# Kernel optimization log

Measured on AMD Instinct MI355X. Metric: run time of the kernel, lower is better.

The kernel has to match this reference:

```python
import jax, jax.numpy as jnp
import numpy as np

BN_EPS = 1e-5

def _tok2img(f):
    # f: [197, 768] tokens (CLS first). Drop CLS, transpose, reshape -> [1, 768, 14, 14].
    # fv4[0, c, i, j] = f[1 + i*14 + j, c], identical to the original triple loop.
    return f[1:].T.reshape(1, 768, 14, 14)

def _resize(x, s):
    # PyTorch F.interpolate(mode='bilinear', align_corners=False) == jax.image.resize 'bilinear'
    n, c, h, w = x.shape
    return jax.image.resize(x, (n, c, h * s, w * s), method='bilinear')

def _conv_relu_bn(x, conv_w, conv_b, g, b, m, v):
    y = jax.lax.conv_general_dilated(x, conv_w, window_strides=(1, 1), padding='SAME',
                                     dimension_numbers=('NCHW', 'OIHW', 'NCHW'))
    y = y + conv_b[None, :, None, None]
    y = jax.nn.relu(y)
    # BatchNorm2d(1) in eval mode with running stats
    scale = g * jax.lax.rsqrt(v + BN_EPS)
    return y * scale[None, :, None, None] + (b - m * scale)[None, :, None, None]

def setup_inputs() -> dict:
    key = jax.random.key(0)
    ks = jax.random.split(key, 4)
    return {
        'x': jax.random.normal(ks[0], (14, 14), dtype=jnp.float32),
        'fv': jax.random.normal(ks[1], (4, 197, 768), dtype=jnp.float32),
        'conv_w': jax.random.normal(ks[2], (1, 769, 3, 3), dtype=jnp.float32) * 0.02,
        'conv_b': jnp.zeros((1,), jnp.float32),
        'bn_gamma': jnp.ones((1,), jnp.float32),
        'bn_beta': jnp.zeros((1,), jnp.float32),
        'bn_mean': jnp.zeros((1,), jnp.float32),
        'bn_var': jnp.ones((1,), jnp.float32),
        'W_w': jax.random.normal(ks[3], (224, 224), dtype=jnp.float32) * 0.05,
        'W_b': jnp.zeros((224,), jnp.float32),
    }

def reference(x, fv, conv_w, conv_b, bn_gamma, bn_beta, bn_mean, bn_var, W_w, W_b):
    h = x[None, None]  # [1,1,14,14]
    # skip features, pre-resized to match current resolution at each stage
    feats = (
        _tok2img(fv[3]),              # 14x14
        _resize(_tok2img(fv[2]), 2),  # 28x28
        _resize(_tok2img(fv[1]), 4),  # 56x56
        _resize(_tok2img(fv[0]), 8),  # 112x112
    )
    for f in feats:
        h = jnp.concatenate([h, f], axis=1)  # [1,769,H,W]
        h = _conv_relu_bn(h, conv_w, conv_b, bn_gamma, bn_beta, bn_mean, bn_var)
        h = _resize(h, 2)
    # Linear(224,224) over the last dim of [1,1,224,224]
    h = jnp.einsum('nchw,ow->ncho', h, W_w) + W_b
    return jax.nn.sigmoid(h)
```

## Files before the change

### kernel.cpp

```cpp
#include <hip/hip_runtime.h>
#include <math.h>


#define BN_EPS 1e-5f

__device__ __forceinline__ float clampf(float x, float lo, float hi) {
    return fminf(fmaxf(x, lo), hi);
}

__device__ __forceinline__ float sampleB(const float* __restrict__ Bt, float fy, float fx) {
    int y0 = (int)fy; float by = fy - (float)y0; int y1 = min(y0 + 1, 13);
    int x0 = (int)fx; float bx = fx - (float)x0; int x1 = min(x0 + 1, 13);
    return (1.f - by) * ((1.f - bx) * Bt[y0 * 14 + x0] + bx * Bt[y0 * 14 + x1])
         + by         * ((1.f - bx) * Bt[y1 * 14 + x0] + bx * Bt[y1 * 14 + x1]);
}

__device__ __forceinline__ float stage_pixel(int i, int j, int H,
                                             const float* __restrict__ hsrc, int srcH,
                                             const float* __restrict__ sB,
                                             const float* __restrict__ cw, float bias) {
    float featScale = 14.0f / (float)H;
    float srcMax = (float)(srcH - 1);
    float acc = bias;

#pragma unroll
    for (int a = 0; a < 3; ++a) {
        int p = i + a - 1;
        if (p < 0 || p >= H) continue;
        float fy = clampf(((float)p + 0.5f) * featScale - 0.5f, 0.f, 13.f);
        float hy = clampf(((float)p + 0.5f) * 0.5f - 0.5f, 0.f, srcMax);
        int hy0 = (int)hy; float fhy = hy - (float)hy0; int hy1 = min(hy0 + 1, srcH - 1);
#pragma unroll
        for (int bq = 0; bq < 3; ++bq) {
            int q = j + bq - 1;
            if (q < 0 || q >= H) continue;
            int t = a * 3 + bq;

            float fx = clampf(((float)q + 0.5f) * featScale - 0.5f, 0.f, 13.f);
            float bv = sampleB(sB + t * 196, fy, fx);

            float hx = clampf(((float)q + 0.5f) * 0.5f - 0.5f, 0.f, srcMax);
            int hx0 = (int)hx; float fhx = hx - (float)hx0; int hx1 = min(hx0 + 1, srcH - 1);
            float hval = (1.f - fhy) * ((1.f - fhx) * hsrc[hy0 * srcH + hx0] + fhx * hsrc[hy0 * srcH + hx1])
                       + fhy         * ((1.f - fhx) * hsrc[hy1 * srcH + hx0] + fhx * hsrc[hy1 * srcH + hx1]);
            acc += cw[t] * hval + bv;
        }
    }
    return acc;
}

__device__ __forceinline__ void srcRange(int dlo, int dhi, int srcH, int& slo, int& shi) {
    int H = 2 * srcH;
    int p0 = max(dlo - 1, 0), p1 = min(dhi + 1, H - 1);
    float h0 = fmaxf(((float)p0 + 0.5f) * 0.5f - 0.5f, 0.f);
    float h1 = fmaxf(((float)p1 + 0.5f) * 0.5f - 0.5f, 0.f);
    slo = (int)h0;
    shi = min((int)h1 + 1, srcH - 1);
}

__device__ __forceinline__ void bRange(int dlo, int dhi, int H, int& lo, int& hi) {
    float sc = 14.f / (float)H;
    int p0 = max(dlo - 1, 0), p1 = min(dhi + 1, H - 1);
    float f0 = clampf(((float)p0 + 0.5f) * sc - 0.5f, 0.f, 13.f);
    float f1 = clampf(((float)p1 + 0.5f) * sc - 0.5f, 0.f, 13.f);
    lo = (int)f0;
    hi = min((int)f1 + 1, 13);
}

__global__ __launch_bounds__(256)
void compute_B_kernel(const float* __restrict__ fv, const float* __restrict__ conv_w,
                      const float* __restrict__ W_w,
                      float* __restrict__ gB, float* __restrict__ gWTf) {
    int blk = blockIdx.x;
    int s = blk / 196;
    int uv = blk % 196;
    const float* fvrow = fv + ((size_t)(3 - s) * 197 + 1 + uv) * 768;
    int tid = threadIdx.x;

    if (tid < 32) {
        int idx = blk * 32 + tid;
        int o = idx % 224, xx = idx / 224;
        float acc = 0.f;
#pragma unroll
        for (int d = -1; d <= 2; ++d) {
            int w = 2 * xx + d;
            if (w < 0 || w > 223) continue;
            float hx = clampf(((float)w + 0.5f) * 0.5f - 0.5f, 0.f, 111.f);
            int xx0 = (int)hx; float fx = hx - (float)xx0; int xx1 = min(xx0 + 1, 111);
            float c = (xx0 == xx ? 1.f - fx : 0.f) + (xx1 == xx ? fx : 0.f);
            acc += c * W_w[o * 224 + w];
        }
        gWTf[xx * 224 + o] = acc;
    }

    float part[9];
#pragma unroll
    for (int t = 0; t < 9; ++t) part[t] = 0.f;
    for (int k = tid; k < 768; k += 256) {
        float fval = fvrow[k];
        const float* w = conv_w + (size_t)(1 + k) * 9;
#pragma unroll
        for (int t = 0; t < 9; ++t) part[t] += fval * w[t];
    }
#pragma unroll
    for (int t = 0; t < 9; ++t) {
#pragma unroll
        for (int off = 32; off > 0; off >>= 1)
            part[t] += __shfl_down(part[t], off, 64);
    }
    __shared__ float red[4][9];
    int wave = tid >> 6, lane = tid & 63;
    if (lane == 0) {
#pragma unroll
        for (int t = 0; t < 9; ++t) red[wave][t] = part[t];
    }
    __syncthreads();
    if (tid < 9)
        gB[s * 1764 + tid * 196 + uv] = red[0][tid] + red[1][tid] + red[2][tid] + red[3][tid];
}

__global__ __launch_bounds__(1024, 1)
void refine_kernel(const float* __restrict__ x,
                   const float* __restrict__ conv_w, const float* __restrict__ conv_b,
                   const float* __restrict__ bng, const float* __restrict__ bnb,
                   const float* __restrict__ bnm, const float* __restrict__ bnv,
                   const float* __restrict__ W_b,
                   const float* __restrict__ gB, const float* __restrict__ gWTf,
                   float* __restrict__ out) {
    __shared__ float sB[4 * 9 * 196];
    __shared__ float y1s[196];
    __shared__ float y2s[784];
    __shared__ float y3s[3136];
    __shared__ float y4loc[3 * 112];
    __shared__ float partial[12 * 224];

    int tid = threadIdx.x;
    int b = blockIdx.x;

    int y4lo = max(b - 1, 0), y4hi = min(b + 1, 111);
    int r3lo, r3hi; srcRange(y4lo, y4hi, 56, r3lo, r3hi);
    int r2lo, r2hi; srcRange(r3lo, r3hi, 28, r2lo, r2hi);
    int r1lo, r1hi; srcRange(r2lo, r2hi, 14, r1lo, r1hi);

    int bl0 = max(r1lo - 1, 0), bh0 = min(r1hi + 1, 13);
    int bl1, bh1; bRange(r2lo, r2hi, 28, bl1, bh1);
    int bl2, bh2; bRange(r3lo, r3hi, 56, bl2, bh2);
    int bl3, bh3; bRange(y4lo, y4hi, 112, bl3, bh3);

    {
        int bl[4] = {bl0, bl1, bl2, bl3}, bh[4] = {bh0, bh1, bh2, bh3};
#pragma unroll
        for (int s4 = 0; s4 < 4; ++s4) {
            int nrw = (bh[s4] - bl[s4] + 1) * 14;
            int n = 9 * nrw;
            int base = s4 * 1764 + bl[s4] * 14;
            for (int e = tid; e < n; e += 1024) {
                int t = e / nrw, rem = e % nrw;
                int off = base + t * 196 + rem;
                sB[off] = gB[off];
            }
        }
    }

    float cw[9];
#pragma unroll
    for (int t = 0; t < 9; ++t) cw[t] = conv_w[t];
    float bias = conv_b[0];
    float scale = bng[0] * rsqrtf(bnv[0] + BN_EPS);
    float shift = bnb[0] - bnm[0] * scale;
    __syncthreads();

    {
        int n = (r1hi - r1lo + 1) * 14;
        if (tid < n) {
            int i = r1lo + tid / 14, j = tid % 14;
            float acc = bias;
#pragma unroll
            for (int a = 0; a < 3; ++a) {
                int p = i + a - 1;
                if (p < 0 || p >= 14) continue;
#pragma unroll
                for (int bq = 0; bq < 3; ++bq) {
                    int q = j + bq - 1;
                    if (q < 0 || q >= 14) continue;
                    int t = a * 3 + bq;
                    acc += cw[t] * x[p * 14 + q] + sB[t * 196 + p * 14 + q];
                }
            }
            y1s[i * 14 + j] = fmaxf(acc, 0.f) * scale + shift;
        }
    }
    __syncthreads();

    {
        int n = (r2hi - r2lo + 1) * 28;
        if (tid < n) {
            int i = r2lo + tid / 28, j = tid % 28;
            float acc = stage_pixel(i, j, 28, y1s, 14, sB + 1764, cw, bias);
            y2s[i * 28 + j] = fmaxf(acc, 0.f) * scale + shift;
        }
    }
    __syncthreads();

    {
        int n = (r3hi - r3lo + 1) * 56;
        if (tid < n) {
            int i = r3lo + tid / 56, j = tid % 56;
            float acc = stage_pixel(i, j, 56, y2s, 28, sB + 2 * 1764, cw, bias);
            y3s[i * 56 + j] = fmaxf(acc, 0.f) * scale + shift;
        }
    }
    __syncthreads();

    {
        int n = (y4hi - y4lo + 1) * 112;
        if (tid < n) {
            int i = y4lo + tid / 112, j = tid % 112;
            float acc = stage_pixel(i, j, 112, y3s, 56, sB + 3 * 1764, cw, bias);
            y4loc[(i - (b - 1)) * 112 + j] = fmaxf(acc, 0.f) * scale + shift;
        }
    }
    __syncthreads();

    if (tid < 896) {
        int kq = tid / 224, o = tid % 224;
        int k0 = kq * 28;
        float a0 = 0.f, a1 = 0.f, a2 = 0.f;
        for (int k = k0; k < k0 + 28; ++k) {
            float wf = gWTf[k * 224 + o];
            a0 += y4loc[k] * wf;
            a1 += y4loc[112 + k] * wf;
            a2 += y4loc[224 + k] * wf;
        }
        partial[(0 * 4 + kq) * 224 + o] = a0;
        partial[(1 * 4 + kq) * 224 + o] = a1;
        partial[(2 * 4 + kq) * 224 + o] = a2;
    }
    __syncthreads();

    if (tid < 448) {
        int rr = tid / 224, o = tid % 224;
        int r = 2 * b + rr;
        float hy = clampf(((float)r + 0.5f) * 0.5f - 0.5f, 0.f, 111.f);
        int yy0 = (int)hy; float fy = hy - (float)yy0; int yy1 = min(yy0 + 1, 111);
        int s0 = yy0 - (b - 1), s1 = yy1 - (b - 1);
        float D0 = partial[(s0 * 4 + 0) * 224 + o] + partial[(s0 * 4 + 1) * 224 + o]
                 + partial[(s0 * 4 + 2) * 224 + o] + partial[(s0 * 4 + 3) * 224 + o];
        float D1 = partial[(s1 * 4 + 0) * 224 + o] + partial[(s1 * 4 + 1) * 224 + o]
                 + partial[(s1 * 4 + 2) * 224 + o] + partial[(s1 * 4 + 3) * 224 + o];
        float v = (1.f - fy) * D0 + fy * D1 + W_b[o];
        out[(size_t)r * 224 + o] = 1.f / (1.f + expf(-v));
    }
}

extern "C" void kernel_launch(void* const* d_in, const int* in_sizes, int n_in,
                              void* d_out, int out_size, void* d_ws, size_t ws_size,
                              hipStream_t stream) {
    (void)in_sizes; (void)n_in; (void)out_size; (void)ws_size;
    const float* x      = (const float*)d_in[0];
    const float* fv     = (const float*)d_in[1];
    const float* conv_w = (const float*)d_in[2];
    const float* conv_b = (const float*)d_in[3];
    const float* bng    = (const float*)d_in[4];
    const float* bnb    = (const float*)d_in[5];
    const float* bnm    = (const float*)d_in[6];
    const float* bnv    = (const float*)d_in[7];
    const float* W_w    = (const float*)d_in[8];
    const float* W_b    = (const float*)d_in[9];
    float* out = (float*)d_out;

    float* ws   = (float*)d_ws;
    float* gB   = ws;
    float* gWTf = ws + 7056;

    compute_B_kernel<<<784, 256, 0, stream>>>(fv, conv_w, W_w, gB, gWTf);
    refine_kernel<<<112, 1024, 0, stream>>>(x, conv_w, conv_b, bng, bnb, bnm, bnv,
                                            W_b, gB, gWTf, out);
}
```

Baseline: 85.89 us.

## Fuse feature projection into refine kernel using bf16 MFMA, drop precompute pass

Removes the separate kernel that projected the skip features onto the conv weights and folded the resize into the Linear weights. Each block now computes only the projection rows it needs, using bf16 MFMA 16x16x32 with conv weights packed in shared memory. The final Linear is applied to an explicitly upsampled row, streaming W_w through shared memory in chunks. This saves a launch and global round-trip but recomputes overlapping projections across blocks, loses precision by rounding to bf16, and has every block re-read all of W_w.

```diff
diff --git a/kernel.cpp b/kernel.cpp
--- a/kernel.cpp
+++ b/kernel.cpp
@@ -4,8 +4,16 @@
 
 #define BN_EPS 1e-5f
 
+typedef __attribute__((ext_vector_type(8))) short bf16x8;
+typedef __attribute__((ext_vector_type(4))) float f32x4;
+
 __device__ __forceinline__ float clampf(float x, float lo, float hi) {
     return fminf(fmaxf(x, lo), hi);
+}
+
+__device__ __forceinline__ unsigned short f2bf(float f) {
+    unsigned u = __float_as_uint(f);
+    return (unsigned short)((u + 0x7FFFu + ((u >> 16) & 1u)) >> 16);
 }
 
 __device__ __forceinline__ float sampleB(const float* __restrict__ Bt, float fy, float fx) {
@@ -22,7 +30,6 @@
     float featScale = 14.0f / (float)H;
     float srcMax = (float)(srcH - 1);
     float acc = bias;
-
 #pragma unroll
     for (int a = 0; a < 3; ++a) {
         int p = i + a - 1;
@@ -35,10 +42,8 @@
             int q = j + bq - 1;
             if (q < 0 || q >= H) continue;
             int t = a * 3 + bq;
-
             float fx = clampf(((float)q + 0.5f) * featScale - 0.5f, 0.f, 13.f);
             float bv = sampleB(sB + t * 196, fy, fx);
-
             float hx = clampf(((float)q + 0.5f) * 0.5f - 0.5f, 0.f, srcMax);
             int hx0 = (int)hx; float fhx = hx - (float)hx0; int hx1 = min(hx0 + 1, srcH - 1);
             float hval = (1.f - fhy) * ((1.f - fhx) * hsrc[hy0 * srcH + hx0] + fhx * hsrc[hy0 * srcH + hx1])
@@ -67,99 +72,67 @@
     hi = min((int)f1 + 1, 13);
 }
 
-__global__ __launch_bounds__(256)
-void compute_B_kernel(const float* __restrict__ fv, const float* __restrict__ conv_w,
-                      const float* __restrict__ W_w,
-                      float* __restrict__ gB, float* __restrict__ gWTf) {
-    int blk = blockIdx.x;
-    int s = blk / 196;
-    int uv = blk % 196;
-    const float* fvrow = fv + ((size_t)(3 - s) * 197 + 1 + uv) * 768;
-    int tid = threadIdx.x;
-
-    if (tid < 32) {
-        int idx = blk * 32 + tid;
-        int o = idx % 224, xx = idx / 224;
-        float acc = 0.f;
-#pragma unroll
-        for (int d = -1; d <= 2; ++d) {
-            int w = 2 * xx + d;
-            if (w < 0 || w > 223) continue;
-            float hx = clampf(((float)w + 0.5f) * 0.5f - 0.5f, 0.f, 111.f);
-            int xx0 = (int)hx; float fx = hx - (float)xx0; int xx1 = min(xx0 + 1, 111);
-            float c = (xx0 == xx ? 1.f - fx : 0.f) + (xx1 == xx ? fx : 0.f);
-            acc += c * W_w[o * 224 + w];
-        }
-        gWTf[xx * 224 + o] = acc;
-    }
-
-    float part[9];
-#pragma unroll
-    for (int t = 0; t < 9; ++t) part[t] = 0.f;
-    for (int k = tid; k < 768; k += 256) {
-        float fval = fvrow[k];
-        const float* w = conv_w + (size_t)(1 + k) * 9;
-#pragma unroll
-        for (int t = 0; t < 9; ++t) part[t] += fval * w[t];
-    }
-#pragma unroll
-    for (int t = 0; t < 9; ++t) {
-#pragma unroll
-        for (int off = 32; off > 0; off >>= 1)
-            part[t] += __shfl_down(part[t], off, 64);
-    }
-    __shared__ float red[4][9];
-    int wave = tid >> 6, lane = tid & 63;
-    if (lane == 0) {
-#pragma unroll
-        for (int t = 0; t < 9; ++t) red[wave][t] = part[t];
-    }
-    __syncthreads();
-    if (tid < 9)
-        gB[s * 1764 + tid * 196 + uv] = red[0][tid] + red[1][tid] + red[2][tid] + red[3][tid];
-}
-
 __global__ __launch_bounds__(1024, 1)
-void refine_kernel(const float* __restrict__ x,
-                   const float* __restrict__ conv_w, const float* __restrict__ conv_b,
-                   const float* __restrict__ bng, const float* __restrict__ bnb,
-                   const float* __restrict__ bnm, const float* __restrict__ bnv,
-                   const float* __restrict__ W_b,
-                   const float* __restrict__ gB, const float* __restrict__ gWTf,
-                   float* __restrict__ out) {
+void refiner_kernel(const float* __restrict__ x, const float* __restrict__ fv,
+                    const float* __restrict__ conv_w, const float* __restrict__ conv_b,
+                    const float* __restrict__ bng, const float* __restrict__ bnb,
+                    const float* __restrict__ bnm, const float* __restrict__ bnv,
+                    const float* __restrict__ W_w, const float* __restrict__ W_b,
+                    float* __restrict__ out) {
     __shared__ float sB[4 * 9 * 196];
-    __shared__ float y1s[196];
-    __shared__ float y2s[784];
-    __shared__ float y3s[3136];
     __shared__ float y4loc[3 * 112];
-    __shared__ float partial[12 * 224];
+    __shared__ float hrow[2 * 224];
+    __shared__ int   pixOff[288];
+    __shared__ int   pixSB[288];
+    __shared__ union {
+        struct { short cbf[24 * 64 * 8]; } ph1;
+        struct { float y1s[196]; float y2s[784]; float y3s[3136]; } ph2;
+        struct { float Wt[32 * 225]; } ph3;
+    } ovl;
 
     int tid = threadIdx.x;
     int b = blockIdx.x;
+    int wv = tid >> 6, lane = tid & 63;
 
     int y4lo = max(b - 1, 0), y4hi = min(b + 1, 111);
     int r3lo, r3hi; srcRange(y4lo, y4hi, 56, r3lo, r3hi);
     int r2lo, r2hi; srcRange(r3lo, r3hi, 28, r2lo, r2hi);
     int r1lo, r1hi; srcRange(r2lo, r2hi, 14, r1lo, r1hi);
 
-    int bl0 = max(r1lo - 1, 0), bh0 = min(r1hi + 1, 13);
-    int bl1, bh1; bRange(r2lo, r2hi, 28, bl1, bh1);
-    int bl2, bh2; bRange(r3lo, r3hi, 56, bl2, bh2);
-    int bl3, bh3; bRange(y4lo, y4hi, 112, bl3, bh3);
-
-    {
-        int bl[4] = {bl0, bl1, bl2, bl3}, bh[4] = {bh0, bh1, bh2, bh3};
-#pragma unroll
-        for (int s4 = 0; s4 < 4; ++s4) {
-            int nrw = (bh[s4] - bl[s4] + 1) * 14;
-            int n = 9 * nrw;
-            int base = s4 * 1764 + bl[s4] * 14;
-            for (int e = tid; e < n; e += 1024) {
-                int t = e / nrw, rem = e % nrw;
-                int off = base + t * 196 + rem;
-                sB[off] = gB[off];
-            }
-        }
+    int bl[4], bh[4];
+    bl[0] = max(r1lo - 1, 0); bh[0] = min(r1hi + 1, 13);
+    bRange(r2lo, r2hi, 28, bl[1], bh[1]);
+    bRange(r3lo, r3hi, 56, bl[2], bh[2]);
+    bRange(y4lo, y4hi, 112, bl[3], bh[3]);
+
+    int start[4], n_p = 0;
+#pragma unroll
+    for (int s = 0; s < 4; ++s) { start[s] = n_p; n_p += (bh[s] - bl[s] + 1) * 14; }
+
+    if (tid < 288) {
+        int p = tid, voff = 0, vsb = 0;
+        if (p < n_p) {
+            int s = (p >= start[1]) + (p >= start[2]) + (p >= start[3]);
+            int loc = p - start[s];
+            int u = bl[s] + loc / 14, v = loc % 14;
+            voff = ((3 - s) * 197 + 1 + u * 14 + v) * 768;
+            vsb  = s * 1764 + u * 14 + v;
+        }
+        pixOff[p] = voff; pixSB[p] = vsb;
+    }
+
+    for (int e = tid; e < 6144; e += 1024) {
+        int j2 = (e * 2) & 7;
+        int ln = (e * 2 >> 3) & 63;
+        int k0 = (e * 2 >> 9);
+        int n = ln & 15, quad = ln >> 4;
+        unsigned lo = 0, hi = 0;
+        if (n < 9) {
+            int k = k0 * 32 + quad * 8 + j2;
+            lo = f2bf(conv_w[(size_t)(1 + k) * 9 + n]);
+            hi = f2bf(conv_w[(size_t)(2 + k) * 9 + n]);
+        }
+        ((unsigned*)ovl.ph1.cbf)[e] = lo | (hi << 16);
     }
 
     float cw[9];
@@ -168,6 +141,36 @@
     float bias = conv_b[0];
     float scale = bng[0] * rsqrtf(bnv[0] + BN_EPS);
     float shift = bnb[0] - bnm[0] * scale;
+    __syncthreads();
+
+    int n_tiles = (n_p + 15) >> 4;
+    for (int mt = wv; mt < n_tiles; mt += 16) {
+        int m0 = mt * 16;
+        int quad = lane >> 4;
+        int mp = min(m0 + (lane & 15), 287);
+        const float* ap = fv + pixOff[mp] + quad * 8;
+        f32x4 c = {0.f, 0.f, 0.f, 0.f};
+#pragma unroll 4
+        for (int k0 = 0; k0 < 24; ++k0) {
+            float4 a0 = *(const float4*)(ap + k0 * 32);
+            float4 a1 = *(const float4*)(ap + k0 * 32 + 4);
+            bf16x8 af;
+            af[0] = (short)f2bf(a0.x); af[1] = (short)f2bf(a0.y);
+            af[2] = (short)f2bf(a0.z); af[3] = (short)f2bf(a0.w);
+            af[4] = (short)f2bf(a1.x); af[5] = (short)f2bf(a1.y);
+            af[6] = (short)f2bf(a1.z); af[7] = (short)f2bf(a1.w);
+            bf16x8 bfr = *(const bf16x8*)&ovl.ph1.cbf[(k0 * 64 + lane) * 8];
+            c = __builtin_amdgcn_mfma_f32_16x16x32_bf16(af, bfr, c, 0, 0, 0);
+        }
+        int t = lane & 15;
+        if (t < 9) {
+#pragma unroll
+            for (int r = 0; r < 4; ++r) {
+                int p = m0 + quad * 4 + r;
+                if (p < n_p) sB[pixSB[p] + t * 196] = c[r];
+            }
+        }
+    }
     __syncthreads();
 
     {
@@ -187,7 +190,7 @@
                     acc += cw[t] * x[p * 14 + q] + sB[t * 196 + p * 14 + q];
                 }
             }
-            y1s[i * 14 + j] = fmaxf(acc, 0.f) * scale + shift;
+            ovl.ph2.y1s[i * 14 + j] = fmaxf(acc, 0.f) * scale + shift;
         }
     }
     __syncthreads();
@@ -196,8 +199,8 @@
         int n = (r2hi - r2lo + 1) * 28;
         if (tid < n) {
             int i = r2lo + tid / 28, j = tid % 28;
-            float acc = stage_pixel(i, j, 28, y1s, 14, sB + 1764, cw, bias);
-            y2s[i * 28 + j] = fmaxf(acc, 0.f) * scale + shift;
+            float acc = stage_pixel(i, j, 28, ovl.ph2.y1s, 14, sB + 1764, cw, bias);
+            ovl.ph2.y2s[i * 28 + j] = fmaxf(acc, 0.f) * scale + shift;
         }
     }
     __syncthreads();
@@ -206,8 +209,8 @@
         int n = (r3hi - r3lo + 1) * 56;
         if (tid < n) {
             int i = r3lo + tid / 56, j = tid % 56;
-            float acc = stage_pixel(i, j, 56, y2s, 28, sB + 2 * 1764, cw, bias);
-            y3s[i * 56 + j] = fmaxf(acc, 0.f) * scale + shift;
+            float acc = stage_pixel(i, j, 56, ovl.ph2.y2s, 28, sB + 2 * 1764, cw, bias);
+            ovl.ph2.y3s[i * 56 + j] = fmaxf(acc, 0.f) * scale + shift;
         }
     }
     __syncthreads();
@@ -216,47 +219,52 @@
         int n = (y4hi - y4lo + 1) * 112;
         if (tid < n) {
             int i = y4lo + tid / 112, j = tid % 112;
-            float acc = stage_pixel(i, j, 112, y3s, 56, sB + 3 * 1764, cw, bias);
+            float acc = stage_pixel(i, j, 112, ovl.ph2.y3s, 56, sB + 3 * 1764, cw, bias);
             y4loc[(i - (b - 1)) * 112 + j] = fmaxf(acc, 0.f) * scale + shift;
         }
     }
     __syncthreads();
 
-    if (tid < 896) {
-        int kq = tid / 224, o = tid % 224;
-        int k0 = kq * 28;
-        float a0 = 0.f, a1 = 0.f, a2 = 0.f;
-        for (int k = k0; k < k0 + 28; ++k) {
-            float wf = gWTf[k * 224 + o];
-            a0 += y4loc[k] * wf;
-            a1 += y4loc[112 + k] * wf;
-            a2 += y4loc[224 + k] * wf;
-        }
-        partial[(0 * 4 + kq) * 224 + o] = a0;
-        partial[(1 * 4 + kq) * 224 + o] = a1;
-        partial[(2 * 4 + kq) * 224 + o] = a2;
-    }
-    __syncthreads();
-
     if (tid < 448) {
-        int rr = tid / 224, o = tid % 224;
+        int rr = tid / 224, w = tid % 224;
         int r = 2 * b + rr;
         float hy = clampf(((float)r + 0.5f) * 0.5f - 0.5f, 0.f, 111.f);
         int yy0 = (int)hy; float fy = hy - (float)yy0; int yy1 = min(yy0 + 1, 111);
+        float hx = clampf(((float)w + 0.5f) * 0.5f - 0.5f, 0.f, 111.f);
+        int xx0 = (int)hx; float fx = hx - (float)xx0; int xx1 = min(xx0 + 1, 111);
         int s0 = yy0 - (b - 1), s1 = yy1 - (b - 1);
-        float D0 = partial[(s0 * 4 + 0) * 224 + o] + partial[(s0 * 4 + 1) * 224 + o]
-                 + partial[(s0 * 4 + 2) * 224 + o] + partial[(s0 * 4 + 3) * 224 + o];
-        float D1 = partial[(s1 * 4 + 0) * 224 + o] + partial[(s1 * 4 + 1) * 224 + o]
-                 + partial[(s1 * 4 + 2) * 224 + o] + partial[(s1 * 4 + 3) * 224 + o];
-        float v = (1.f - fy) * D0 + fy * D1 + W_b[o];
-        out[(size_t)r * 224 + o] = 1.f / (1.f + expf(-v));
+        hrow[rr * 224 + w] = (1.f - fy) * ((1.f - fx) * y4loc[s0 * 112 + xx0] + fx * y4loc[s0 * 112 + xx1])
+                           + fy         * ((1.f - fx) * y4loc[s1 * 112 + xx0] + fx * y4loc[s1 * 112 + xx1]);
+    }
+
+    float a0 = 0.f, a1 = 0.f;
+    for (int c = 0; c < 7; ++c) {
+        __syncthreads();
+        for (int e = tid; e < 7168; e += 1024) {
+            int o = e >> 5, wl = e & 31;
+            ovl.ph3.Wt[wl * 225 + o] = W_w[o * 224 + (c << 5) + wl];
+        }
+        __syncthreads();
+        if (tid < 224) {
+#pragma unroll 8
+            for (int wl = 0; wl < 32; ++wl) {
+                float wvv = ovl.ph3.Wt[wl * 225 + tid];
+                a0 += hrow[(c << 5) + wl] * wvv;
+                a1 += hrow[224 + (c << 5) + wl] * wvv;
+            }
+        }
+    }
+    if (tid < 224) {
+        float v0 = a0 + W_b[tid], v1 = a1 + W_b[tid];
+        out[(size_t)(2 * b) * 224 + tid]     = 1.f / (1.f + expf(-v0));
+        out[(size_t)(2 * b + 1) * 224 + tid] = 1.f / (1.f + expf(-v1));
     }
 }
 
 extern "C" void kernel_launch(void* const* d_in, const int* in_sizes, int n_in,
                               void* d_out, int out_size, void* d_ws, size_t ws_size,
                               hipStream_t stream) {
-    (void)in_sizes; (void)n_in; (void)out_size; (void)ws_size;
+    (void)in_sizes; (void)n_in; (void)out_size; (void)d_ws; (void)ws_size;
     const float* x      = (const float*)d_in[0];
     const float* fv     = (const float*)d_in[1];
     const float* conv_w = (const float*)d_in[2];
@@ -269,11 +277,6 @@
     const float* W_b    = (const float*)d_in[9];
     float* out = (float*)d_out;
 
-    float* ws   = (float*)d_ws;
-    float* gB   = ws;
-    float* gWTf = ws + 7056;
-
-    compute_B_kernel<<<784, 256, 0, stream>>>(fv, conv_w, W_w, gB, gWTf);
-    refine_kernel<<<112, 1024, 0, stream>>>(x, conv_w, conv_b, bng, bnb, bnm, bnv,
-                                            W_b, gB, gWTf, out);
-}
+    refiner_kernel<<<112, 1024, 0, stream>>>(x, fv, conv_w, conv_b,
+                                             bng, bnb, bnm, bnv, W_w, W_b, out);
+}
```

After: 113.6 us. 1.32x slower.

## Precompute column-interpolated skip-feature projections and shrink refine-kernel shared windows

Applied to the files above, without the earlier changes.

The feature-projection kernel now runs 56 blocks of 1024 threads, each handling one row of 14 tokens. It splits the 768-channel dot products across 8 slices, reduces them in shared memory, and applies the horizontal bilinear resize before writing a per-stage, per-tap table at full width. The refine kernel then needs only a 1D vertical interpolation of that table, and it stages only the row windows it needs into smaller shared buffers. This cuts per-pixel interpolation work and LDS footprint. In exchange it writes a larger intermediate table and launches far fewer blocks in the first kernel, each doing strided conv_w reads.

```diff
diff --git a/kernel.cpp b/kernel.cpp
--- a/kernel.cpp
+++ b/kernel.cpp
@@ -6,47 +6,6 @@
 
 __device__ __forceinline__ float clampf(float x, float lo, float hi) {
     return fminf(fmaxf(x, lo), hi);
-}
-
-__device__ __forceinline__ float sampleB(const float* __restrict__ Bt, float fy, float fx) {
-    int y0 = (int)fy; float by = fy - (float)y0; int y1 = min(y0 + 1, 13);
-    int x0 = (int)fx; float bx = fx - (float)x0; int x1 = min(x0 + 1, 13);
-    return (1.f - by) * ((1.f - bx) * Bt[y0 * 14 + x0] + bx * Bt[y0 * 14 + x1])
-         + by         * ((1.f - bx) * Bt[y1 * 14 + x0] + bx * Bt[y1 * 14 + x1]);
-}
-
-__device__ __forceinline__ float stage_pixel(int i, int j, int H,
-                                             const float* __restrict__ hsrc, int srcH,
-                                             const float* __restrict__ sB,
-                                             const float* __restrict__ cw, float bias) {
-    float featScale = 14.0f / (float)H;
-    float srcMax = (float)(srcH - 1);
-    float acc = bias;
-
-#pragma unroll
-    for (int a = 0; a < 3; ++a) {
-        int p = i + a - 1;
-        if (p < 0 || p >= H) continue;
-        float fy = clampf(((float)p + 0.5f) * featScale - 0.5f, 0.f, 13.f);
-        float hy = clampf(((float)p + 0.5f) * 0.5f - 0.5f, 0.f, srcMax);
-        int hy0 = (int)hy; float fhy = hy - (float)hy0; int hy1 = min(hy0 + 1, srcH - 1);
-#pragma unroll
-        for (int bq = 0; bq < 3; ++bq) {
-            int q = j + bq - 1;
-            if (q < 0 || q >= H) continue;
-            int t = a * 3 + bq;
-
-            float fx = clampf(((float)q + 0.5f) * featScale - 0.5f, 0.f, 13.f);
-            float bv = sampleB(sB + t * 196, fy, fx);
-
-            float hx = clampf(((float)q + 0.5f) * 0.5f - 0.5f, 0.f, srcMax);
-            int hx0 = (int)hx; float fhx = hx - (float)hx0; int hx1 = min(hx0 + 1, srcH - 1);
-            float hval = (1.f - fhy) * ((1.f - fhx) * hsrc[hy0 * srcH + hx0] + fhx * hsrc[hy0 * srcH + hx1])
-                       + fhy         * ((1.f - fhx) * hsrc[hy1 * srcH + hx0] + fhx * hsrc[hy1 * srcH + hx1]);
-            acc += cw[t] * hval + bv;
-        }
-    }
-    return acc;
 }
 
 __device__ __forceinline__ void srcRange(int dlo, int dhi, int srcH, int& slo, int& shi) {
@@ -67,18 +26,22 @@
     hi = min((int)f1 + 1, 13);
 }
 
-__global__ __launch_bounds__(256)
+__constant__ int kW[4] = {14, 28, 56, 112};
+__constant__ int kG[4] = {0, 1764, 5292, 12348};
+
+__global__ __launch_bounds__(1024)
 void compute_B_kernel(const float* __restrict__ fv, const float* __restrict__ conv_w,
                       const float* __restrict__ W_w,
-                      float* __restrict__ gB, float* __restrict__ gWTf) {
-    int blk = blockIdx.x;
-    int s = blk / 196;
-    int uv = blk % 196;
-    const float* fvrow = fv + ((size_t)(3 - s) * 197 + 1 + uv) * 768;
+                      float* __restrict__ gBt, float* __restrict__ gWTf) {
+    __shared__ float part[1008];
+    __shared__ float sbrow[126];
+
+    int b = blockIdx.x;
+    int s = b / 14, u = b % 14;
     int tid = threadIdx.x;
 
-    if (tid < 32) {
-        int idx = blk * 32 + tid;
+    if (tid < 448) {
+        int idx = b * 448 + tid;
         int o = idx % 224, xx = idx / 224;
         float acc = 0.f;
 #pragma unroll
@@ -93,30 +56,74 @@
         gWTf[xx * 224 + o] = acc;
     }
 
-    float part[9];
-#pragma unroll
-    for (int t = 0; t < 9; ++t) part[t] = 0.f;
-    for (int k = tid; k < 768; k += 256) {
-        float fval = fvrow[k];
-        const float* w = conv_w + (size_t)(1 + k) * 9;
-#pragma unroll
-        for (int t = 0; t < 9; ++t) part[t] += fval * w[t];
-    }
-#pragma unroll
-    for (int t = 0; t < 9; ++t) {
-#pragma unroll
-        for (int off = 32; off > 0; off >>= 1)
-            part[t] += __shfl_down(part[t], off, 64);
-    }
-    __shared__ float red[4][9];
-    int wave = tid >> 6, lane = tid & 63;
-    if (lane == 0) {
-#pragma unroll
-        for (int t = 0; t < 9; ++t) red[wave][t] = part[t];
-    }
-    __syncthreads();
-    if (tid < 9)
-        gB[s * 1764 + tid * 196 + uv] = red[0][tid] + red[1][tid] + red[2][tid] + red[3][tid];
+    if (tid < 1008) {
+        int p = tid / 72, r = tid % 72;
+        int sl = r / 9, t = r % 9;
+        const float* fvrow = fv + ((size_t)(3 - s) * 197 + 1 + u * 14 + p) * 768 + sl * 96;
+        const float* cwp = conv_w + (size_t)(1 + sl * 96) * 9 + t;
+        float acc = 0.f;
+#pragma unroll 32
+        for (int m = 0; m < 96; ++m)
+            acc += fvrow[m] * cwp[m * 9];
+        part[(p * 9 + t) * 8 + sl] = acc;
+    }
+    __syncthreads();
+
+    if (tid < 126) {
+        float v = 0.f;
+        int base = tid * 8;
+#pragma unroll
+        for (int k = 0; k < 8; ++k) v += part[base + k];
+        sbrow[tid] = v;
+    }
+    __syncthreads();
+
+    int W = kW[s], G = kG[s];
+    int n = 9 * W;
+    if (tid < n) {
+        int t = tid / W, q = tid % W;
+        float sc = 14.f / (float)W;
+        float fx = clampf(((float)q + 0.5f) * sc - 0.5f, 0.f, 13.f);
+        int x0 = (int)fx; float f = fx - (float)x0; int x1 = min(x0 + 1, 13);
+        float val = (1.f - f) * sbrow[x0 * 9 + t] + f * sbrow[x1 * 9 + t];
+        gBt[G + (t * 14 + u) * W + q] = val;
+    }
+}
+
+__device__ __forceinline__ float stage_px(int i, int j, int H, int srcH,
+                                          const float* __restrict__ hsrc, int srcLo,
+                                          const float* __restrict__ cB, int nr, int bLo,
+                                          const float* __restrict__ cw, float bias) {
+    float featScale = 14.f / (float)H;
+    float srcMax = (float)(srcH - 1);
+    float acc = bias;
+#pragma unroll
+    for (int a = 0; a < 3; ++a) {
+        int p = i + a - 1;
+        if (p < 0 || p >= H) continue;
+        float fy = clampf(((float)p + 0.5f) * featScale - 0.5f, 0.f, 13.f);
+        int by0 = (int)fy; float byf = fy - (float)by0; int by1 = min(by0 + 1, 13);
+        const float* b0 = cB + (by0 - bLo) * H;
+        const float* b1 = cB + (by1 - bLo) * H;
+        float hy = clampf(((float)p + 0.5f) * 0.5f - 0.5f, 0.f, srcMax);
+        int hy0 = (int)hy; float fhy = hy - (float)hy0; int hy1 = min(hy0 + 1, srcH - 1);
+        const float* h0 = hsrc + (hy0 - srcLo) * srcH;
+        const float* h1 = hsrc + (hy1 - srcLo) * srcH;
+#pragma unroll
+        for (int bq = 0; bq < 3; ++bq) {
+            int q = j + bq - 1;
+            if (q < 0 || q >= H) continue;
+            int t = a * 3 + bq;
+            int toff = t * nr * H;
+            float bv = (1.f - byf) * b0[toff + q] + byf * b1[toff + q];
+            float hx = clampf(((float)q + 0.5f) * 0.5f - 0.5f, 0.f, srcMax);
+            int hx0 = (int)hx; float fhx = hx - (float)hx0; int hx1 = min(hx0 + 1, srcH - 1);
+            float hval = (1.f - fhy) * ((1.f - fhx) * h0[hx0] + fhx * h0[hx1])
+                       + fhy         * ((1.f - fhx) * h1[hx0] + fhx * h1[hx1]);
+            acc += cw[t] * hval + bv;
+        }
+    }
+    return acc;
 }
 
 __global__ __launch_bounds__(1024, 1)
@@ -125,12 +132,15 @@
                    const float* __restrict__ bng, const float* __restrict__ bnb,
                    const float* __restrict__ bnm, const float* __restrict__ bnv,
                    const float* __restrict__ W_b,
-                   const float* __restrict__ gB, const float* __restrict__ gWTf,
+                   const float* __restrict__ gBt, const float* __restrict__ gWTf,
                    float* __restrict__ out) {
-    __shared__ float sB[4 * 9 * 196];
-    __shared__ float y1s[196];
-    __shared__ float y2s[784];
-    __shared__ float y3s[3136];
+    __shared__ float cB0[9 * 9 * 14];
+    __shared__ float cB1[9 * 7 * 28];
+    __shared__ float cB2[9 * 5 * 56];
+    __shared__ float cB3[9 * 4 * 112];
+    __shared__ float y1w[9 * 14];
+    __shared__ float y2w[7 * 28];
+    __shared__ float y3w[6 * 56];
     __shared__ float y4loc[3 * 112];
     __shared__ float partial[12 * 224];
 
@@ -146,20 +156,26 @@
     int bl1, bh1; bRange(r2lo, r2hi, 28, bl1, bh1);
     int bl2, bh2; bRange(r3lo, r3hi, 56, bl2, bh2);
     int bl3, bh3; bRange(y4lo, y4hi, 112, bl3, bh3);
-
-    {
-        int bl[4] = {bl0, bl1, bl2, bl3}, bh[4] = {bh0, bh1, bh2, bh3};
-#pragma unroll
-        for (int s4 = 0; s4 < 4; ++s4) {
-            int nrw = (bh[s4] - bl[s4] + 1) * 14;
-            int n = 9 * nrw;
-            int base = s4 * 1764 + bl[s4] * 14;
-            for (int e = tid; e < n; e += 1024) {
-                int t = e / nrw, rem = e % nrw;
-                int off = base + t * 196 + rem;
-                sB[off] = gB[off];
-            }
-        }
+    int nr0 = min(bh0 - bl0 + 1, 9);
+    int nr1 = min(bh1 - bl1 + 1, 7);
+    int nr2 = min(bh2 - bl2 + 1, 5);
+    int nr3 = min(bh3 - bl3 + 1, 4);
+
+    {
+        int m = nr0 * 14, n = 9 * m, base = kG[0] + bl0 * 14;
+        for (int e = tid; e < n; e += 1024) { int t = e / m; cB0[e] = gBt[base + t * 196 + (e - t * m)]; }
+    }
+    {
+        int m = nr1 * 28, n = 9 * m, base = kG[1] + bl1 * 28;
+        for (int e = tid; e < n; e += 1024) { int t = e / m; cB1[e] = gBt[base + t * 392 + (e - t * m)]; }
+    }
+    {
+        int m = nr2 * 56, n = 9 * m, base = kG[2] + bl2 * 56;
+        for (int e = tid; e < n; e += 1024) { int t = e / m; cB2[e] = gBt[base + t * 784 + (e - t * m)]; }
+    }
+    {
+        int m = nr3 * 112, n = 9 * m, base = kG[3] + bl3 * 112;
+        for (int e = tid; e < n; e += 1024) { int t = e / m; cB3[e] = gBt[base + t * 1568 + (e - t * m)]; }
     }
 
     float cw[9];
@@ -184,10 +200,10 @@
                     int q = j + bq - 1;
                     if (q < 0 || q >= 14) continue;
                     int t = a * 3 + bq;
-                    acc += cw[t] * x[p * 14 + q] + sB[t * 196 + p * 14 + q];
+                    acc += cw[t] * x[p * 14 + q] + cB0[(t * nr0 + (p - bl0)) * 14 + q];
                 }
             }
-            y1s[i * 14 + j] = fmaxf(acc, 0.f) * scale + shift;
+            y1w[(i - r1lo) * 14 + j] = fmaxf(acc, 0.f) * scale + shift;
         }
     }
     __syncthreads();
@@ -196,8 +212,8 @@
         int n = (r2hi - r2lo + 1) * 28;
         if (tid < n) {
             int i = r2lo + tid / 28, j = tid % 28;
-            float acc = stage_pixel(i, j, 28, y1s, 14, sB + 1764, cw, bias);
-            y2s[i * 28 + j] = fmaxf(acc, 0.f) * scale + shift;
+            float acc = stage_px(i, j, 28, 14, y1w, r1lo, cB1, nr1, bl1, cw, bias);
+            y2w[(i - r2lo) * 28 + j] = fmaxf(acc, 0.f) * scale + shift;
         }
     }
     __syncthreads();
@@ -206,8 +222,8 @@
         int n = (r3hi - r3lo + 1) * 56;
         if (tid < n) {
             int i = r3lo + tid / 56, j = tid % 56;
-            float acc = stage_pixel(i, j, 56, y2s, 28, sB + 2 * 1764, cw, bias);
-            y3s[i * 56 + j] = fmaxf(acc, 0.f) * scale + shift;
+            float acc = stage_px(i, j, 56, 28, y2w, r2lo, cB2, nr2, bl2, cw, bias);
+            y3w[(i - r3lo) * 56 + j] = fmaxf(acc, 0.f) * scale + shift;
         }
     }
     __syncthreads();
@@ -216,8 +232,8 @@
         int n = (y4hi - y4lo + 1) * 112;
         if (tid < n) {
             int i = y4lo + tid / 112, j = tid % 112;
-            float acc = stage_pixel(i, j, 112, y3s, 56, sB + 3 * 1764, cw, bias);
-            y4loc[(i - (b - 1)) * 112 + j] = fmaxf(acc, 0.f) * scale + shift;
+            float acc = stage_px(i, j, 112, 56, y3w, r3lo, cB3, nr3, bl3, cw, bias);
+            y4loc[(i - y4lo) * 112 + j] = fmaxf(acc, 0.f) * scale + shift;
         }
     }
     __syncthreads();
@@ -243,7 +259,7 @@
         int r = 2 * b + rr;
         float hy = clampf(((float)r + 0.5f) * 0.5f - 0.5f, 0.f, 111.f);
         int yy0 = (int)hy; float fy = hy - (float)yy0; int yy1 = min(yy0 + 1, 111);
-        int s0 = yy0 - (b - 1), s1 = yy1 - (b - 1);
+        int s0 = yy0 - y4lo, s1 = yy1 - y4lo;
         float D0 = partial[(s0 * 4 + 0) * 224 + o] + partial[(s0 * 4 + 1) * 224 + o]
                  + partial[(s0 * 4 + 2) * 224 + o] + partial[(s0 * 4 + 3) * 224 + o];
         float D1 = partial[(s1 * 4 + 0) * 224 + o] + partial[(s1 * 4 + 1) * 224 + o]
@@ -270,10 +286,10 @@
     float* out = (float*)d_out;
 
     float* ws   = (float*)d_ws;
-    float* gB   = ws;
-    float* gWTf = ws + 7056;
-
-    compute_B_kernel<<<784, 256, 0, stream>>>(fv, conv_w, W_w, gB, gWTf);
+    float* gBt  = ws;
+    float* gWTf = ws + 26460;
+
+    compute_B_kernel<<<56, 1024, 0, stream>>>(fv, conv_w, W_w, gBt, gWTf);
     refine_kernel<<<112, 1024, 0, stream>>>(x, conv_w, conv_b, bng, bnb, bnm, bnv,
-                                            W_b, gB, gWTf, out);
-}
+                                            W_b, gBt, gWTf, out);
+}
```

Result: slower. 104.4 us (+21.5%).
